# Optimization experiments

Hardware: AMD Instinct MI355X
Metric: run time of the kernel (lower is better)

Reference implementation:

```python
import jax, jax.numpy as jnp
import numpy as np

B, LQ, DIM, NH, NPTS, NL = 8, 9216, 384, 6, 4, 1
HD = DIM // NH            # 64 per head
H0, W0 = 96, 96           # single-level feature map, LKV = 9216
LN_EPS = 1e-5

def layer_norm(x, w, b):
    mu = jnp.mean(x, -1, keepdims=True)
    var = jnp.var(x, -1, keepdims=True)
    return (x - mu) * jax.lax.rsqrt(var + LN_EPS) * w + b

def ms_deform_attn_core(value, spatial_shapes_np, loc, attw):
    # value: [B, LKV, NH, HD]; loc: [B, LQ, NH, NL, NPTS, 2] normalized in [0,1]
    # attw:  [B, LQ, NH, NL, NPTS] (softmaxed over NL*NPTS)
    Bv, _, nH, d = value.shape
    Lq = loc.shape[1]
    per_level = []
    start = 0
    for lvl, (H, W) in enumerate(spatial_shapes_np):
        H, W = int(H), int(W)
        v = jnp.transpose(value[:, start:start + H * W], (0, 2, 1, 3))  # [B,NH,HW,HD]
        start += H * W
        ploc = loc[:, :, :, lvl]                      # [B,LQ,NH,NPTS,2]
        # grid_sample(mode=bilinear, padding=zeros, align_corners=False) pixel coords
        x = ploc[..., 0] * W - 0.5
        y = ploc[..., 1] * H - 0.5
        x0 = jnp.floor(x)
        y0 = jnp.floor(y)
        acc = jnp.zeros((Bv, nH, Lq * NPTS, d), value.dtype)
        for dx in (0.0, 1.0):
            for dy in (0.0, 1.0):
                xi = x0 + dx
                yi = y0 + dy
                w_bil = (1.0 - jnp.abs(x - xi)) * (1.0 - jnp.abs(y - yi))
                valid = (xi >= 0) & (xi < W) & (yi >= 0) & (yi < H)
                idx = (jnp.clip(yi, 0, H - 1) * W + jnp.clip(xi, 0, W - 1)).astype(jnp.int32)
                idx = jnp.transpose(idx, (0, 2, 1, 3)).reshape(Bv, nH, Lq * NPTS)
                g = jnp.take_along_axis(v, idx[..., None], axis=2)  # [B,NH,LQ*NPTS,HD]
                wv = jnp.transpose(w_bil * valid, (0, 2, 1, 3)).reshape(Bv, nH, Lq * NPTS, 1)
                acc = acc + g * wv
        per_level.append(acc.reshape(Bv, nH, Lq, NPTS, d))
    samp = jnp.stack(per_level, axis=3)               # [B,NH,LQ,NL,NPTS,HD]
    aw = jnp.transpose(attw, (0, 2, 1, 3, 4))         # [B,NH,LQ,NL,NPTS]
    out = jnp.einsum('bhqlpd,bhqlp->bqhd', samp, aw)
    return out.reshape(Bv, Lq, nH * d)

def _forward(query, reference_points, feat, spatial_shapes_np,
             qn_w, qn_b, fn_w, fn_b, w_value, b_value, w_off, b_off,
             w_attn, b_attn, w_out, b_out, gamma):
    q = layer_norm(query, qn_w, qn_b)
    f = layer_norm(feat, fn_w, fn_b)
    value = (f @ w_value + b_value).reshape(B, -1, NH, HD)
    off = (q @ w_off + b_off).reshape(B, LQ, NH, NL, NPTS, 2)
    attw = jax.nn.softmax((q @ w_attn + b_attn).reshape(B, LQ, NH, NL * NPTS), -1)
    attw = attw.reshape(B, LQ, NH, NL, NPTS)
    # offset_normalizer = (W, H) per level
    norm = jnp.asarray(np.ascontiguousarray(spatial_shapes_np[:, ::-1]), jnp.float32)
    loc = reference_points[:, :, None, :, None, :] + off / norm[None, None, None, :, None, :]
    attn_out = ms_deform_attn_core(value, spatial_shapes_np, loc, attw)
    attn_out = attn_out @ w_out + b_out
    return query + gamma * attn_out

def setup_inputs():
    key = jax.random.key(0)
    ks = jax.random.split(key, 16)
    s = 0.02
    return {
        "query": jax.random.normal(ks[0], (B, LQ, DIM), jnp.float32),
        "reference_points": jax.random.uniform(ks[1], (B, LQ, NL, 2), dtype=jnp.float32),
        "feat": jax.random.normal(ks[2], (B, H0 * W0, DIM), jnp.float32),
        "spatial_shapes": jnp.array([[H0, W0]], jnp.int32),
        "level_start_index": jnp.array([0], jnp.int32),
        "qn_w": jnp.ones((DIM,), jnp.float32),
        "qn_b": jnp.zeros((DIM,), jnp.float32),
        "fn_w": jnp.ones((DIM,), jnp.float32),
        "fn_b": jnp.zeros((DIM,), jnp.float32),
        "w_value": s * jax.random.normal(ks[3], (DIM, DIM), jnp.float32),
        "b_value": jnp.zeros((DIM,), jnp.float32),
        "w_off": s * jax.random.normal(ks[4], (DIM, NH * NL * NPTS * 2), jnp.float32),
        "b_off": 0.5 * jax.random.normal(ks[5], (NH * NL * NPTS * 2,), jnp.float32),
        "w_attn": s * jax.random.normal(ks[6], (DIM, NH * NL * NPTS), jnp.float32),
        "b_attn": jnp.zeros((NH * NL * NPTS,), jnp.float32),
        "w_out": s * jax.random.normal(ks[7], (DIM, DIM), jnp.float32),
        "b_out": jnp.zeros((DIM,), jnp.float32),
        "gamma": 0.1 * jax.random.normal(ks[8], (DIM,), jnp.float32),
    }

def reference(query, reference_points, feat, spatial_shapes, level_start_index,
              qn_w, qn_b, fn_w, fn_b, w_value, b_value, w_off, b_off,
              w_attn, b_attn, w_out, b_out, gamma):
    ss = np.asarray(spatial_shapes)
    return _forward(query, reference_points, feat, ss,
                    qn_w, qn_b, fn_w, fn_b, w_value, b_value, w_off, b_off,
                    w_attn, b_attn, w_out, b_out, gamma)
```

## Files before the change

### kernel.cpp

```cpp
#include <hip/hip_runtime.h>
#include <hip/hip_bf16.h>
#include <math.h>

#define Bsz   8
#define LQ    9216
#define DIM   384
#define NH    6
#define NPTS  4
#define HD    64
#define H0    96
#define W0    96
#define NROWS (Bsz * LQ)
#define LN_EPS 1e-5f

typedef __attribute__((ext_vector_type(8))) short short8;
typedef __attribute__((ext_vector_type(4))) float f32x4;

__device__ __forceinline__ void load_lds16(const void* g, void* l) {
    __builtin_amdgcn_global_load_lds(
        (const __attribute__((address_space(1))) void*)g,
        (__attribute__((address_space(3))) void*)l,
        16, 0, 0);
}

__device__ __forceinline__ float bf_lo(unsigned u) { return __uint_as_float(u << 16); }
__device__ __forceinline__ float bf_hi(unsigned u) { return __uint_as_float(u & 0xffff0000u); }

__device__ __forceinline__ int xcd_swizzle(int orig, int nwg) {
    int q = nwg >> 3, r = nwg & 7;
    int xcd = orig & 7, idx = orig >> 3;
    int base = (xcd < r) ? xcd * (q + 1) : r * (q + 1) + (xcd - r) * q;
    return base + idx;
}

__global__ __launch_bounds__(256) void lnorm_kernel(
    const float* __restrict__ X,
    const float* __restrict__ w, const float* __restrict__ bvec,
    __hip_bfloat16* __restrict__ Y)
{
    int wave = threadIdx.x >> 6, lane = threadIdx.x & 63;
    int row = blockIdx.x * 4 + wave;
    const float* x = X + (size_t)row * DIM;
    float2 v[3];
    float s = 0.f, sq = 0.f;
#pragma unroll
    for (int i = 0; i < 3; ++i) {
        v[i] = *(const float2*)&x[lane * 2 + i * 128];
        s  += v[i].x + v[i].y;
        sq += v[i].x * v[i].x + v[i].y * v[i].y;
    }
#pragma unroll
    for (int off = 1; off < 64; off <<= 1) {
        s  += __shfl_xor(s,  off, 64);
        sq += __shfl_xor(sq, off, 64);
    }
    float mu   = s * (1.f / DIM);
    float rstd = rsqrtf(sq * (1.f / DIM) - mu * mu + LN_EPS);
#pragma unroll
    for (int i = 0; i < 3; ++i) {
        int p = lane * 2 + i * 128;
        float2 ww = *(const float2*)&w[p];
        float2 bb = *(const float2*)&bvec[p];
        __hip_bfloat162 o;
        o.x = __float2bfloat16((v[i].x - mu) * rstd * ww.x + bb.x);
        o.y = __float2bfloat16((v[i].y - mu) * rstd * ww.y + bb.y);
        *(__hip_bfloat162*)&Y[(size_t)row * DIM + p] = o;
    }
}

__global__ __launch_bounds__(256) void wtrans_kernel(
    const float* __restrict__ wv, const float* __restrict__ wo,
    const float* __restrict__ woff, const float* __restrict__ watt,
    __hip_bfloat16* __restrict__ WtV, __hip_bfloat16* __restrict__ WtO,
    __hip_bfloat16* __restrict__ WtS)
{
    int gid = blockIdx.x * 256 + threadIdx.x;
    if (gid < 147456) {
        int n = gid / 384, k = gid % 384;
        WtV[gid] = __float2bfloat16(wv[k * 384 + n]);
    } else if (gid < 294912) {
        int i = gid - 147456;
        int n = i / 384, k = i % 384;
        WtO[i] = __float2bfloat16(wo[k * 384 + n]);
    } else {
        int i = gid - 294912;
        int n = i / 384, k = i % 384;
        float v = 0.f;
        if (n < 48)      v = woff[k * 48 + n];
        else if (n < 72) v = watt[k * 24 + (n - 48)];
        WtS[i] = __float2bfloat16(v);
    }
}

template<int MODE>
__global__ __launch_bounds__(256) void gemm16_kernel(
    const __hip_bfloat16* __restrict__ A,
    const __hip_bfloat16* __restrict__ Bt,
    const float* __restrict__ bias,
    const float* __restrict__ bias2,
    const float* __restrict__ resid,
    const float* __restrict__ gamma,
    void* __restrict__ out0,
    void* __restrict__ out1)
{
    __shared__ short As[128 * 32];
    __shared__ short Bs[128 * 32];

    const int t    = threadIdx.x;
    const int lane = t & 63;
    const int w    = t >> 6;
    const int wm   = w >> 1, wn = w & 1;

    const int nwg  = gridDim.x * gridDim.y;
    const int wg   = xcd_swizzle(blockIdx.y * gridDim.x + blockIdx.x, nwg);
    const int row0 = (wg / gridDim.x) * 128;
    const int col0 = (wg % gridDim.x) * 128;
    const int lm   = lane & 15, lq = lane >> 4;

    f32x4 acc[4][4];
#pragma unroll
    for (int i = 0; i < 4; ++i)
#pragma unroll
        for (int j = 0; j < 4; ++j)
            acc[i][j] = (f32x4){0.f, 0.f, 0.f, 0.f};

    for (int k0 = 0; k0 < 384; k0 += 32) {
#pragma unroll
        for (int j = 0; j < 2; ++j) {
            int seg = w * 2 + j;
            int rr  = seg * 16 + (lane >> 2);
            const char* gA = (const char*)(A  + ((size_t)(row0 + rr) * 384 + k0)) + (lane & 3) * 16;
            const char* gB = (const char*)(Bt + ((size_t)(col0 + rr) * 384 + k0)) + (lane & 3) * 16;
            load_lds16(gA, (char*)As + seg * 1024);
            load_lds16(gB, (char*)Bs + seg * 1024);
        }
        __syncthreads();

        short8 af[4], bf[4];
#pragma unroll
        for (int i = 0; i < 4; ++i) {
            af[i] = *(const short8*)&As[(wm * 64 + i * 16 + lm) * 32 + lq * 8];
            bf[i] = *(const short8*)&Bs[(wn * 64 + i * 16 + lm) * 32 + lq * 8];
        }
#pragma unroll
        for (int i = 0; i < 4; ++i)
#pragma unroll
            for (int j = 0; j < 4; ++j)
                acc[i][j] = __builtin_amdgcn_mfma_f32_16x16x32_bf16(af[i], bf[j], acc[i][j], 0, 0, 0);
        __syncthreads();
    }

#pragma unroll
    for (int i = 0; i < 4; ++i) {
#pragma unroll
        for (int j = 0; j < 4; ++j) {
            const int col = col0 + wn * 64 + j * 16 + lm;
#pragma unroll
            for (int r = 0; r < 4; ++r) {
                const int row = row0 + wm * 64 + i * 16 + lq * 4 + r;
                float v = acc[i][j][r];
                if (MODE == 0) {
                    v += bias[col];
                    int b = row / LQ, pix = row - b * LQ;
                    int h = col >> 6, d = col & 63;
                    ((__hip_bfloat16*)out0)[(((size_t)(b * NH + h)) * LQ + pix) * 64 + d] =
                        __float2bfloat16(v);
                } else if (MODE == 1) {
                    v += bias[col];
                    size_t o = (size_t)row * 384 + col;
                    ((float*)out0)[o] = resid[o] + gamma[col] * v;
                } else {
                    if (col < 48)
                        ((float*)out0)[(size_t)row * 48 + col] = v + bias[col];
                    else if (col < 72)
                        ((float*)out1)[(size_t)row * 24 + (col - 48)] = v + bias2[col - 48];
                }
            }
        }
    }
}

__global__ __launch_bounds__(256) void locsoftmax_kernel(
    const float* __restrict__ offbuf, const float* __restrict__ attbuf,
    const float* __restrict__ refpts, float4* __restrict__ smp)
{
    int gid = blockIdx.x * blockDim.x + threadIdx.x;
    int row = gid / NH;
    int h   = gid % NH;
    int b   = row / LQ, q = row - b * LQ;
    size_t task = (size_t)(b * NH + h) * LQ + q;

    const float rx = refpts[row * 2 + 0];
    const float ry = refpts[row * 2 + 1];

    const float* off = offbuf + (size_t)row * (NH * NPTS * 2) + h * (NPTS * 2);
    const float* att = attbuf + (size_t)row * (NH * NPTS)     + h * NPTS;

    float l0 = att[0], l1 = att[1], l2 = att[2], l3 = att[3];
    float m  = fmaxf(fmaxf(l0, l1), fmaxf(l2, l3));
    float e[4] = {expf(l0 - m), expf(l1 - m), expf(l2 - m), expf(l3 - m)};
    float inv = 1.f / (e[0] + e[1] + e[2] + e[3]);

#pragma unroll
    for (int p = 0; p < NPTS; ++p) {
        float x = (rx + off[p * 2 + 0] * (1.f / W0)) * (float)W0 - 0.5f;
        float y = (ry + off[p * 2 + 1] * (1.f / H0)) * (float)H0 - 0.5f;
        smp[task * 4 + p] = make_float4(x, y, e[p] * inv, 0.f);
    }
}

__global__ __launch_bounds__(256) void sample_kernel(
    const __hip_bfloat16* __restrict__ vt,
    const float4* __restrict__ smp,
    __hip_bfloat16* __restrict__ out)
{
    const int wave = threadIdx.x >> 6, lane = threadIdx.x & 63;
    const int slot = lane >> 4;
    const int c4   = lane & 15;
    const int wg   = xcd_swizzle(blockIdx.x, gridDim.x);
    const int task = (wg * 4 + wave) * 4 + slot;
    const int bh   = task / LQ;
    const int q    = task - bh * LQ;
    const int b    = bh / NH, h = bh - b * NH;

    const __hip_bfloat16* vbase = vt + (size_t)bh * LQ * 64;

    float a0 = 0.f, a1 = 0.f, a2 = 0.f, a3 = 0.f;

#pragma unroll
    for (int p = 0; p < NPTS; ++p) {
        float4 s = smp[(size_t)task * 4 + p];
        float x = s.x, y = s.y, wgt = s.z;
        float xf = floorf(x), yf = floorf(y);
        int   x0 = (int)xf,   y0 = (int)yf;
        float fx = x - xf,    fy = y - yf;
        float gx0 = 1.f - fx, gx1 = fx;
        float gy0w = (1.f - fy) * wgt, gy1w = fy * wgt;

#pragma unroll
        for (int cy = 0; cy < 2; ++cy) {
            const int   yi = y0 + cy;
            const float wy = cy ? gy1w : gy0w;
            const bool  vy = (unsigned)yi < H0;
            const int   yc = min(max(yi, 0), H0 - 1);
#pragma unroll
            for (int cx = 0; cx < 2; ++cx) {
                const int xi = x0 + cx;
                float wc = wy * (cx ? gx1 : gx0);
                if (!vy || (unsigned)xi >= W0) wc = 0.f;
                const int xc = min(max(xi, 0), W0 - 1);
                const uint2 raw = *(const uint2*)(vbase + (size_t)(yc * W0 + xc) * 64 + c4 * 4);
                a0 = fmaf(wc, bf_lo(raw.x), a0);
                a1 = fmaf(wc, bf_hi(raw.x), a1);
                a2 = fmaf(wc, bf_lo(raw.y), a2);
                a3 = fmaf(wc, bf_hi(raw.y), a3);
            }
        }
    }

    const int row = b * LQ + q;
    __hip_bfloat162 o01, o23;
    o01.x = __float2bfloat16(a0); o01.y = __float2bfloat16(a1);
    o23.x = __float2bfloat16(a2); o23.y = __float2bfloat16(a3);
    __hip_bfloat162* op = (__hip_bfloat162*)(out + (size_t)row * DIM + h * HD + c4 * 4);
    op[0] = o01;
    op[1] = o23;
}

extern "C" void kernel_launch(void* const* d_in, const int* in_sizes, int n_in,
                              void* d_out, int out_size, void* d_ws, size_t ws_size,
                              hipStream_t stream)
{
    const float* query   = (const float*)d_in[0];
    const float* refpts  = (const float*)d_in[1];
    const float* feat    = (const float*)d_in[2];
    const float* qn_w    = (const float*)d_in[5];
    const float* qn_b    = (const float*)d_in[6];
    const float* fn_w    = (const float*)d_in[7];
    const float* fn_b    = (const float*)d_in[8];
    const float* w_value = (const float*)d_in[9];
    const float* b_value = (const float*)d_in[10];
    const float* w_off   = (const float*)d_in[11];
    const float* b_off   = (const float*)d_in[12];
    const float* w_attn  = (const float*)d_in[13];
    const float* b_attn  = (const float*)d_in[14];
    const float* w_out   = (const float*)d_in[15];
    const float* b_out   = (const float*)d_in[16];
    const float* gamma   = (const float*)d_in[17];

    char* wsb = (char*)d_ws;
    __hip_bfloat16* Q16    = (__hip_bfloat16*)wsb;
    __hip_bfloat16* F16    = (__hip_bfloat16*)(wsb + 56623104);
    __hip_bfloat16* vtrans = (__hip_bfloat16*)(wsb + 113246208);
    __hip_bfloat16* att16  = (__hip_bfloat16*)(wsb + 169869312);
    float*          offbuf = (float*)(wsb + 226492416);
    float*          attbuf = (float*)(wsb + 240648192);
    __hip_bfloat16* WtV    = (__hip_bfloat16*)(wsb + 247726080);
    __hip_bfloat16* WtO    = (__hip_bfloat16*)(wsb + 248020992);
    __hip_bfloat16* WtS    = (__hip_bfloat16*)(wsb + 248315904);
    float4*         smp    = (float4*)wsb;
    float* outp = (float*)d_out;

    lnorm_kernel<<<NROWS / 4, 256, 0, stream>>>(query, qn_w, qn_b, Q16);
    lnorm_kernel<<<NROWS / 4, 256, 0, stream>>>(feat,  fn_w, fn_b, F16);

    wtrans_kernel<<<1344, 256, 0, stream>>>(w_value, w_out, w_off, w_attn,
                                            WtV, WtO, WtS);

    gemm16_kernel<0><<<dim3(3, NROWS / 128), 256, 0, stream>>>(
        F16, WtV, b_value, nullptr, nullptr, nullptr, vtrans, nullptr);

    gemm16_kernel<2><<<dim3(1, NROWS / 128), 256, 0, stream>>>(
        Q16, WtS, b_off, b_attn, nullptr, nullptr, offbuf, attbuf);

    locsoftmax_kernel<<<(NROWS * NH) / 256, 256, 0, stream>>>(
        offbuf, attbuf, refpts, smp);

    sample_kernel<<<(NROWS * NH) / 16, 256, 0, stream>>>(
        vtrans, smp, att16);

    gemm16_kernel<1><<<dim3(3, NROWS / 128), 256, 0, stream>>>(
        att16, WtO, b_out, nullptr, query, gamma, outp, nullptr);
}
```

Before: 536.4 us.

## Merge front kernels, co-launch value/offset GEMMs, fold softmax into sampler

Both layer norms and the weight transposes now run in one launch. The value-projection and offset/attention GEMMs share a single grid, and the location and softmax computation moves into the sampling kernel, so the smp buffer is never written or read back. This cuts kernel launches and tail gaps, and removes one intermediate round-trip through memory. In exchange, each sample thread recomputes the softmax with scattered small reads, and merged grids can have uneven block costs.

```diff
diff --git a/kernel.cpp b/kernel.cpp
--- a/kernel.cpp
+++ b/kernel.cpp
@@ -33,13 +33,13 @@
     return base + idx;
 }
 
-__global__ __launch_bounds__(256) void lnorm_kernel(
+__device__ __forceinline__ void ln_rows(
     const float* __restrict__ X,
     const float* __restrict__ w, const float* __restrict__ bvec,
-    __hip_bfloat16* __restrict__ Y)
+    __hip_bfloat16* __restrict__ Y, int blk)
 {
     int wave = threadIdx.x >> 6, lane = threadIdx.x & 63;
-    int row = blockIdx.x * 4 + wave;
+    int row = blk * 4 + wave;
     const float* x = X + (size_t)row * DIM;
     float2 v[3];
     float s = 0.f, sq = 0.f;
@@ -68,32 +68,44 @@
     }
 }
 
-__global__ __launch_bounds__(256) void wtrans_kernel(
+__global__ __launch_bounds__(256) void front_kernel(
+    const float* __restrict__ query, const float* __restrict__ qn_w,
+    const float* __restrict__ qn_b, __hip_bfloat16* __restrict__ Q16,
+    const float* __restrict__ feat, const float* __restrict__ fn_w,
+    const float* __restrict__ fn_b, __hip_bfloat16* __restrict__ F16,
     const float* __restrict__ wv, const float* __restrict__ wo,
     const float* __restrict__ woff, const float* __restrict__ watt,
     __hip_bfloat16* __restrict__ WtV, __hip_bfloat16* __restrict__ WtO,
     __hip_bfloat16* __restrict__ WtS)
 {
-    int gid = blockIdx.x * 256 + threadIdx.x;
-    if (gid < 147456) {
-        int n = gid / 384, k = gid % 384;
-        WtV[gid] = __float2bfloat16(wv[k * 384 + n]);
-    } else if (gid < 294912) {
-        int i = gid - 147456;
-        int n = i / 384, k = i % 384;
-        WtO[i] = __float2bfloat16(wo[k * 384 + n]);
+    const int bid = blockIdx.x;
+    if (bid < 18432) {
+        ln_rows(query, qn_w, qn_b, Q16, bid);
+    } else if (bid < 36864) {
+        ln_rows(feat, fn_w, fn_b, F16, bid - 18432);
     } else {
-        int i = gid - 294912;
-        int n = i / 384, k = i % 384;
-        float v = 0.f;
-        if (n < 48)      v = woff[k * 48 + n];
-        else if (n < 72) v = watt[k * 24 + (n - 48)];
-        WtS[i] = __float2bfloat16(v);
+        int gid = (bid - 36864) * 256 + threadIdx.x;
+        if (gid < 147456) {
+            int n = gid / 384, k = gid % 384;
+            WtV[gid] = __float2bfloat16(wv[k * 384 + n]);
+        } else if (gid < 294912) {
+            int i = gid - 147456;
+            int n = i / 384, k = i % 384;
+            WtO[i] = __float2bfloat16(wo[k * 384 + n]);
+        } else {
+            int i = gid - 294912;
+            int n = i / 384, k = i % 384;
+            float v = 0.f;
+            if (n < 48)      v = woff[k * 48 + n];
+            else if (n < 72) v = watt[k * 24 + (n - 48)];
+            WtS[i] = __float2bfloat16(v);
+        }
     }
 }
 
 template<int MODE>
-__global__ __launch_bounds__(256) void gemm16_kernel(
+__device__ __forceinline__ void gemm_body(
+    short* __restrict__ As, short* __restrict__ Bs,
     const __hip_bfloat16* __restrict__ A,
     const __hip_bfloat16* __restrict__ Bt,
     const float* __restrict__ bias,
@@ -101,20 +113,13 @@
     const float* __restrict__ resid,
     const float* __restrict__ gamma,
     void* __restrict__ out0,
-    void* __restrict__ out1)
-{
-    __shared__ short As[128 * 32];
-    __shared__ short Bs[128 * 32];
-
+    void* __restrict__ out1,
+    int row0, int col0)
+{
     const int t    = threadIdx.x;
     const int lane = t & 63;
     const int w    = t >> 6;
     const int wm   = w >> 1, wn = w & 1;
-
-    const int nwg  = gridDim.x * gridDim.y;
-    const int wg   = xcd_swizzle(blockIdx.y * gridDim.x + blockIdx.x, nwg);
-    const int row0 = (wg / gridDim.x) * 128;
-    const int col0 = (wg % gridDim.x) * 128;
     const int lm   = lane & 15, lq = lane >> 4;
 
     f32x4 acc[4][4];
@@ -180,38 +185,50 @@
     }
 }
 
-__global__ __launch_bounds__(256) void locsoftmax_kernel(
-    const float* __restrict__ offbuf, const float* __restrict__ attbuf,
-    const float* __restrict__ refpts, float4* __restrict__ smp)
-{
-    int gid = blockIdx.x * blockDim.x + threadIdx.x;
-    int row = gid / NH;
-    int h   = gid % NH;
-    int b   = row / LQ, q = row - b * LQ;
-    size_t task = (size_t)(b * NH + h) * LQ + q;
-
-    const float rx = refpts[row * 2 + 0];
-    const float ry = refpts[row * 2 + 1];
-
-    const float* off = offbuf + (size_t)row * (NH * NPTS * 2) + h * (NPTS * 2);
-    const float* att = attbuf + (size_t)row * (NH * NPTS)     + h * NPTS;
-
-    float l0 = att[0], l1 = att[1], l2 = att[2], l3 = att[3];
-    float m  = fmaxf(fmaxf(l0, l1), fmaxf(l2, l3));
-    float e[4] = {expf(l0 - m), expf(l1 - m), expf(l2 - m), expf(l3 - m)};
-    float inv = 1.f / (e[0] + e[1] + e[2] + e[3]);
-
-#pragma unroll
-    for (int p = 0; p < NPTS; ++p) {
-        float x = (rx + off[p * 2 + 0] * (1.f / W0)) * (float)W0 - 0.5f;
-        float y = (ry + off[p * 2 + 1] * (1.f / H0)) * (float)H0 - 0.5f;
-        smp[task * 4 + p] = make_float4(x, y, e[p] * inv, 0.f);
-    }
+__global__ __launch_bounds__(256) void gemm02_kernel(
+    const __hip_bfloat16* __restrict__ F16, const __hip_bfloat16* __restrict__ WtV,
+    const float* __restrict__ b_value, __hip_bfloat16* __restrict__ vtrans,
+    const __hip_bfloat16* __restrict__ Q16, const __hip_bfloat16* __restrict__ WtS,
+    const float* __restrict__ b_off, const float* __restrict__ b_attn,
+    float* __restrict__ offbuf, float* __restrict__ attbuf)
+{
+    __shared__ short As[128 * 32];
+    __shared__ short Bs[128 * 32];
+    const int wg = xcd_swizzle(blockIdx.x, 2304);
+    if (wg < 1728) {
+        gemm_body<0>(As, Bs, F16, WtV, b_value, nullptr, nullptr, nullptr,
+                     vtrans, nullptr, (wg / 3) * 128, (wg % 3) * 128);
+    } else {
+        const int w2 = wg - 1728;
+        gemm_body<2>(As, Bs, Q16, WtS, b_off, b_attn, nullptr, nullptr,
+                     offbuf, attbuf, w2 * 128, 0);
+    }
+}
+
+template<int MODE>
+__global__ __launch_bounds__(256) void gemm16_kernel(
+    const __hip_bfloat16* __restrict__ A,
+    const __hip_bfloat16* __restrict__ Bt,
+    const float* __restrict__ bias,
+    const float* __restrict__ bias2,
+    const float* __restrict__ resid,
+    const float* __restrict__ gamma,
+    void* __restrict__ out0,
+    void* __restrict__ out1)
+{
+    __shared__ short As[128 * 32];
+    __shared__ short Bs[128 * 32];
+    const int nwg = gridDim.x * gridDim.y;
+    const int wg  = xcd_swizzle(blockIdx.y * gridDim.x + blockIdx.x, nwg);
+    gemm_body<MODE>(As, Bs, A, Bt, bias, bias2, resid, gamma, out0, out1,
+                    (wg / gridDim.x) * 128, (wg % gridDim.x) * 128);
 }
 
 __global__ __launch_bounds__(256) void sample_kernel(
     const __hip_bfloat16* __restrict__ vt,
-    const float4* __restrict__ smp,
+    const float* __restrict__ offbuf,
+    const float* __restrict__ attbuf,
+    const float* __restrict__ refpts,
     __hip_bfloat16* __restrict__ out)
 {
     const int wave = threadIdx.x >> 6, lane = threadIdx.x & 63;
@@ -222,15 +239,26 @@
     const int bh   = task / LQ;
     const int q    = task - bh * LQ;
     const int b    = bh / NH, h = bh - b * NH;
+    const int row  = b * LQ + q;
 
     const __hip_bfloat16* vbase = vt + (size_t)bh * LQ * 64;
 
+    const float* att = attbuf + (size_t)row * (NH * NPTS)     + h * NPTS;
+    const float* off = offbuf + (size_t)row * (NH * NPTS * 2) + h * (NPTS * 2);
+    const float rx = refpts[row * 2 + 0];
+    const float ry = refpts[row * 2 + 1];
+    float l0 = att[0], l1 = att[1], l2 = att[2], l3 = att[3];
+    float m  = fmaxf(fmaxf(l0, l1), fmaxf(l2, l3));
+    float e[4] = {expf(l0 - m), expf(l1 - m), expf(l2 - m), expf(l3 - m)};
+    float inv = 1.f / (e[0] + e[1] + e[2] + e[3]);
+
     float a0 = 0.f, a1 = 0.f, a2 = 0.f, a3 = 0.f;
 
 #pragma unroll
     for (int p = 0; p < NPTS; ++p) {
-        float4 s = smp[(size_t)task * 4 + p];
-        float x = s.x, y = s.y, wgt = s.z;
+        float x   = (rx + off[p * 2 + 0] * (1.f / W0)) * (float)W0 - 0.5f;
+        float y   = (ry + off[p * 2 + 1] * (1.f / H0)) * (float)H0 - 0.5f;
+        float wgt = e[p] * inv;
         float xf = floorf(x), yf = floorf(y);
         int   x0 = (int)xf,   y0 = (int)yf;
         float fx = x - xf,    fy = y - yf;
@@ -258,7 +286,6 @@
         }
     }
 
-    const int row = b * LQ + q;
     __hip_bfloat162 o01, o23;
     o01.x = __float2bfloat16(a0); o01.y = __float2bfloat16(a1);
     o23.x = __float2bfloat16(a2); o23.y = __float2bfloat16(a3);
@@ -298,26 +325,17 @@
     __hip_bfloat16* WtV    = (__hip_bfloat16*)(wsb + 247726080);
     __hip_bfloat16* WtO    = (__hip_bfloat16*)(wsb + 248020992);
     __hip_bfloat16* WtS    = (__hip_bfloat16*)(wsb + 248315904);
-    float4*         smp    = (float4*)wsb;
     float* outp = (float*)d_out;
 
-    lnorm_kernel<<<NROWS / 4, 256, 0, stream>>>(query, qn_w, qn_b, Q16);
-    lnorm_kernel<<<NROWS / 4, 256, 0, stream>>>(feat,  fn_w, fn_b, F16);
-
-    wtrans_kernel<<<1344, 256, 0, stream>>>(w_value, w_out, w_off, w_attn,
-                                            WtV, WtO, WtS);
-
-    gemm16_kernel<0><<<dim3(3, NROWS / 128), 256, 0, stream>>>(
-        F16, WtV, b_value, nullptr, nullptr, nullptr, vtrans, nullptr);
-
-    gemm16_kernel<2><<<dim3(1, NROWS / 128), 256, 0, stream>>>(
-        Q16, WtS, b_off, b_attn, nullptr, nullptr, offbuf, attbuf);
-
-    locsoftmax_kernel<<<(NROWS * NH) / 256, 256, 0, stream>>>(
-        offbuf, attbuf, refpts, smp);
+    front_kernel<<<38208, 256, 0, stream>>>(
+        query, qn_w, qn_b, Q16, feat, fn_w, fn_b, F16,
+        w_value, w_out, w_off, w_attn, WtV, WtO, WtS);
+
+    gemm02_kernel<<<2304, 256, 0, stream>>>(
+        F16, WtV, b_value, vtrans, Q16, WtS, b_off, b_attn, offbuf, attbuf);
 
     sample_kernel<<<(NROWS * NH) / 16, 256, 0, stream>>>(
-        vtrans, smp, att16);
+        vtrans, offbuf, attbuf, refpts, att16);
 
     gemm16_kernel<1><<<dim3(3, NROWS / 128), 256, 0, stream>>>(
         att16, WtO, b_out, nullptr, query, gamma, outp, nullptr);
```

After: 584.7 us. 1.09x slower.
